# Optimization experiments

Measured on AMD Instinct MI355X. Metric: run time of the kernel, lower is better.

Reference implementation:

```python
import jax, jax.numpy as jnp
import numpy as np

DIM = 1024
N_HEAD = 16
HEAD_DIM = DIM // N_HEAD
SCALE = HEAD_DIM ** (-0.5)


def setup_inputs() -> dict:
    key = jax.random.key(0)
    ks = jax.random.split(key, 5)
    x = jax.random.normal(ks[0], (2, 2048, DIM), dtype=jnp.float32)
    # Linear params (torch nn.Linear stores weight as [out, in]; we keep [in, out])
    wqkv = jax.random.normal(ks[1], (DIM, 3 * DIM), dtype=jnp.float32) / np.sqrt(DIM)
    bqkv = jax.random.normal(ks[2], (3 * DIM,), dtype=jnp.float32) * 0.01
    wo = jax.random.normal(ks[3], (DIM, DIM), dtype=jnp.float32) / np.sqrt(DIM)
    bo = jax.random.normal(ks[4], (DIM,), dtype=jnp.float32) * 0.01
    return {"x": x, "wqkv": wqkv, "bqkv": bqkv, "wo": wo, "bo": bo}


def reference(x, wqkv, bqkv, wo, bo):
    b, s, _ = x.shape
    qkv = x @ wqkv + bqkv                      # [b, s, 3*dim]
    q, k, v = jnp.split(qkv, 3, axis=-1)
    # [b, s, h, d] -> [b, h, s, d]
    def heads(t):
        return t.reshape(b, s, N_HEAD, HEAD_DIM).transpose(0, 2, 1, 3)
    q, k, v = heads(q) * SCALE, heads(k), heads(v)
    attn = jnp.einsum('bhqd,bhkd->bhqk', q, k)  # [b, h, s, s]
    attn = jax.nn.softmax(attn, axis=-1)
    out = jnp.einsum('bhqk,bhkd->bhqd', attn, v)
    out = out.transpose(0, 2, 1, 3).reshape(b, s, DIM)
    return out @ wo + bo
```

## Files before the change

kernel.cpp:

```cpp
#include <hip/hip_runtime.h>
#include <hip/hip_bf16.h>

#define DIM   1024
#define NHEAD 16
#define HDIM  64
#define BATCH 2
#define SEQ   2048
#define TOK   (BATCH*SEQ)
#define QSCALE 0.1803368801111204f

typedef unsigned short u16;
typedef __attribute__((ext_vector_type(8))) _Float16 h16x8;
typedef __attribute__((ext_vector_type(2))) __fp16 fp16x2;
typedef __attribute__((ext_vector_type(4))) float f32x4;
typedef __attribute__((ext_vector_type(16))) float f32x16;
typedef __attribute__((ext_vector_type(2))) int i32x2;

__device__ __forceinline__ u16 f2h(float f) {
    union { _Float16 h; u16 u; } v; v.h = (_Float16)f;
    return v.u;
}
__device__ __forceinline__ unsigned pack2h(float a, float b) {
    return (unsigned)f2h(a) | ((unsigned)f2h(b) << 16);
}
__device__ __forceinline__ unsigned pkrtz(float a, float b) {
    union { fp16x2 h; unsigned u; } v;
    v.h = __builtin_amdgcn_cvt_pkrtz(a, b);
    return v.u;
}
__device__ __forceinline__ f32x16 zero16() {
    f32x16 v;
#pragma unroll
    for (int i = 0; i < 16; ++i) v[i] = 0.f;
    return v;
}

typedef __attribute__((address_space(3))) void lds_void;
typedef const __attribute__((address_space(1))) void gbl_void;
__device__ __forceinline__ void gload_lds16(const void* g, void* l) {
    __builtin_amdgcn_global_load_lds((gbl_void*)g, (lds_void*)l, 16, 0, 0);
}

__global__ __launch_bounds__(256)
void fused_cvt(const float* __restrict__ x,    u16* __restrict__ xh,
               const float* __restrict__ wqkv, u16* __restrict__ wqT,
               const float* __restrict__ wo,   u16* __restrict__ woT) {
    __shared__ float t[32][33];
    const int bid = blockIdx.x;
    if (bid < 4096) {
        int i = bid * 256 + threadIdx.x;
        float4 v = ((const float4*)x)[i];
        ((uint2*)xh)[i] = make_uint2(pack2h(v.x, v.y), pack2h(v.z, v.w));
        return;
    }
    const float* in; u16* outT; int K, N, tb;
    if (bid < 7168) { in = wqkv; outT = wqT; K = 1024; N = 3072; tb = bid - 4096; }
    else            { in = wo;   outT = woT; K = 1024; N = 1024; tb = bid - 7168; }
    const int nbx = N / 32;
    const int n0 = (tb % nbx) * 32, k0 = (tb / nbx) * 32;
    const int tx = threadIdx.x & 31, ty = threadIdx.x >> 5;
#pragma unroll
    for (int i = 0; i < 4; ++i)
        t[ty + i * 8][tx] = in[(size_t)(k0 + ty + i * 8) * N + n0 + tx];
    __syncthreads();
#pragma unroll
    for (int i = 0; i < 4; ++i)
        outT[(size_t)(n0 + ty + i * 8) * K + k0 + tx] = f2h(t[tx][ty + i * 8]);
}

__global__ __launch_bounds__(512)
void gemm_qkv(const u16* __restrict__ Ag, const u16* __restrict__ Bg,
              const float* __restrict__ bias, u16* __restrict__ Qh,
              u16* __restrict__ Kh, u16* __restrict__ Vh, int K, int N) {
    __shared__ u16 As[128 * 64];
    __shared__ u16 Bs[128 * 64];

    const int tid  = threadIdx.x;
    const int lane = tid & 63;
    const int w    = tid >> 6;
    const int c    = lane & 15;
    const int quad = lane >> 4;
    const int wm   = (w & 3) * 32;
    const int wn   = (w >> 2) * 64;
    const int row0 = blockIdx.y * 128;
    const int col0 = blockIdx.x * 128;
    const int sw   = c & 7;

    f32x4 acc[2][4];
#pragma unroll
    for (int m = 0; m < 2; ++m)
#pragma unroll
        for (int n = 0; n < 4; ++n) acc[m][n] = (f32x4){0.f, 0.f, 0.f, 0.f};

    for (int k0 = 0; k0 < K; k0 += 64) {
        __syncthreads();
#pragma unroll
        for (int i = 0; i < 2; ++i) {
            int idx = tid + i * 512;
            int r = idx >> 3, p = idx & 7;
            int g = p ^ (r & 7);
            gload_lds16(Ag + (size_t)(row0 + r) * K + k0 + g * 8, &As[idx * 8]);
            gload_lds16(Bg + (size_t)(col0 + r) * K + k0 + g * 8, &Bs[idx * 8]);
        }
        __syncthreads();

        h16x8 af[2][2];
#pragma unroll
        for (int m = 0; m < 2; ++m)
#pragma unroll
            for (int kh = 0; kh < 2; ++kh)
                af[m][kh] = *(const h16x8*)&As[(wm + m * 16 + c) * 64 +
                                              ((kh * 4 + quad) ^ sw) * 8];
#pragma unroll
        for (int kh = 0; kh < 2; ++kh)
#pragma unroll
            for (int n = 0; n < 4; ++n) {
                h16x8 bf = *(const h16x8*)&Bs[(wn + n * 16 + c) * 64 +
                                              ((kh * 4 + quad) ^ sw) * 8];
#pragma unroll
                for (int m = 0; m < 2; ++m)
                    acc[m][n] = __builtin_amdgcn_mfma_f32_16x16x32_f16(
                        af[m][kh], bf, acc[m][n], 0, 0, 0);
            }
    }

#pragma unroll
    for (int n = 0; n < 4; ++n) {
        const int col = col0 + wn + n * 16 + c;
        const float bv = bias[col];
        const int h = (col >> 6) & 15, d = col & 63;
#pragma unroll
        for (int m = 0; m < 2; ++m) {
            const int rbase = row0 + wm + m * 16 + quad * 4;
            const int b = rbase >> 11, s0 = rbase & (SEQ - 1);
            const int bh = (b << 4) + h;
            if (col0 < DIM) {
#pragma unroll
                for (int r = 0; r < 4; ++r)
                    Qh[((size_t)bh * SEQ + s0 + r) * 64 + d] =
                        f2h((acc[m][n][r] + bv) * QSCALE);
            } else if (col0 < 2 * DIM) {
#pragma unroll
                for (int r = 0; r < 4; ++r)
                    Kh[((size_t)bh * SEQ + s0 + r) * 64 + d] =
                        f2h(acc[m][n][r] + bv);
            } else {
                uint2 pv = make_uint2(pack2h(acc[m][n][0] + bv, acc[m][n][1] + bv),
                                      pack2h(acc[m][n][2] + bv, acc[m][n][3] + bv));
                *(uint2*)&Vh[((size_t)bh * 64 + d) * SEQ + s0] = pv;
            }
        }
    }
}

__global__ __launch_bounds__(512)
void gemm_out(const u16* __restrict__ Ag, const u16* __restrict__ Bg,
              const float* __restrict__ bias, float* __restrict__ Cout,
              int M, int N, int K) {
    __shared__ u16 As[128 * 64];
    __shared__ u16 Bs[128 * 64];

    const int tid  = threadIdx.x;
    const int lane = tid & 63;
    const int w    = tid >> 6;
    const int c    = lane & 15;
    const int quad = lane >> 4;
    const int wm   = (w & 3) * 32;
    const int wn   = (w >> 2) * 64;
    const int row0 = blockIdx.y * 128;
    const int col0 = blockIdx.x * 128;
    const int sw   = c & 7;

    f32x4 acc[2][4];
#pragma unroll
    for (int m = 0; m < 2; ++m)
#pragma unroll
        for (int n = 0; n < 4; ++n) acc[m][n] = (f32x4){0.f, 0.f, 0.f, 0.f};

    for (int k0 = 0; k0 < K; k0 += 64) {
        __syncthreads();
#pragma unroll
        for (int i = 0; i < 2; ++i) {
            int idx = tid + i * 512;
            int r = idx >> 3, p = idx & 7;
            int g = p ^ (r & 7);
            gload_lds16(Ag + (size_t)(row0 + r) * K + k0 + g * 8, &As[idx * 8]);
            gload_lds16(Bg + (size_t)(col0 + r) * K + k0 + g * 8, &Bs[idx * 8]);
        }
        __syncthreads();

        h16x8 af[2][2];
#pragma unroll
        for (int m = 0; m < 2; ++m)
#pragma unroll
            for (int kh = 0; kh < 2; ++kh)
                af[m][kh] = *(const h16x8*)&As[(wm + m * 16 + c) * 64 +
                                              ((kh * 4 + quad) ^ sw) * 8];
#pragma unroll
        for (int kh = 0; kh < 2; ++kh)
#pragma unroll
            for (int n = 0; n < 4; ++n) {
                h16x8 bf = *(const h16x8*)&Bs[(wn + n * 16 + c) * 64 +
                                              ((kh * 4 + quad) ^ sw) * 8];
#pragma unroll
                for (int m = 0; m < 2; ++m)
                    acc[m][n] = __builtin_amdgcn_mfma_f32_16x16x32_f16(
                        af[m][kh], bf, acc[m][n], 0, 0, 0);
            }
    }

#pragma unroll
    for (int n = 0; n < 4; ++n) {
        const int col = col0 + wn + n * 16 + c;
        const float bv = bias[col];
#pragma unroll
        for (int m = 0; m < 2; ++m) {
            const int rbase = row0 + wm + m * 16 + quad * 4;
#pragma unroll
            for (int r = 0; r < 4; ++r)
                Cout[(size_t)(rbase + r) * N + col] = acc[m][n][r] + bv;
        }
    }
}

__global__ __launch_bounds__(256, 2)
void flash_attn11(const u16* __restrict__ Qg, const u16* __restrict__ Kg,
                  const u16* __restrict__ Vg, u16* __restrict__ aout) {
    __shared__ u16 Qs[128 * 64];
    __shared__ u16 Ks[2][128 * 64];
    __shared__ u16 Vt[2][64 * 128];

    const int tid  = threadIdx.x;
    const int lane = tid & 63;
    const int w    = tid >> 6;
    const int wq   = w & 1;
    const int wk   = w >> 1;
    const int n32  = lane & 31;
    const int q5   = lane >> 5;
    const int bh   = blockIdx.y;
    const int q0   = blockIdx.x * 128;

    const u16* Qb = Qg + (size_t)bh * SEQ * 64;
    const u16* Kb = Kg + (size_t)bh * SEQ * 64;
    const u16* Vb = Vg + (size_t)bh * 64 * SEQ;

#pragma unroll
    for (int i = 0; i < 4; ++i) {
        int idx = tid + i * 256;
        int r = idx >> 3, p = idx & 7, g = p ^ (r & 7);
        gload_lds16(Qb + (size_t)(q0 + r) * 64 + g * 8, &Qs[idx * 8]);
    }
#pragma unroll
    for (int i = 0; i < 4; ++i) {
        int idx = tid + i * 256;
        int rk = idx >> 3, pk = idx & 7, gk = pk ^ (rk & 7);
        gload_lds16(Kb + (size_t)rk * 64 + gk * 8, &Ks[0][idx * 8]);
        int rv = idx >> 4, cv = idx & 15, gv = cv ^ (rv & 7);
        gload_lds16(Vb + (size_t)rv * SEQ + gv * 8, &Vt[0][idx * 8]);
    }
    __syncthreads();

    const int qrowA = wq * 64 + n32;
    const int qrowB = qrowA + 32;
    const int sw    = n32 & 7;
    h16x8 qbA[4], qbB[4];
#pragma unroll
    for (int s = 0; s < 4; ++s) {
        const int ch = ((s * 2 + q5) ^ sw) * 8;
        qbA[s] = *(const h16x8*)&Qs[qrowA * 64 + ch];
        qbB[s] = *(const h16x8*)&Qs[qrowB * 64 + ch];
    }

    float lA = 0.f, lB = 0.f;
    f32x16 oA[2] = {zero16(), zero16()};
    f32x16 oB[2] = {zero16(), zero16()};

    for (int kt = 0; kt < SEQ / 128; ++kt) {
        const int cur = kt & 1, nxt = cur ^ 1;

        if (kt < SEQ / 128 - 1) {
            const int k1 = (kt + 1) * 128;
#pragma unroll
            for (int i = 0; i < 4; ++i) {
                int idx = tid + i * 256;
                int rk = idx >> 3, pk = idx & 7, gk = pk ^ (rk & 7);
                gload_lds16(Kb + (size_t)(k1 + rk) * 64 + gk * 8, &Ks[nxt][idx * 8]);
                int rv = idx >> 4, cv = idx & 15, gv = cv ^ (rv & 7);
                gload_lds16(Vb + (size_t)rv * SEQ + k1 + gv * 8, &Vt[nxt][idx * 8]);
            }
        }

        unsigned xwA[8][2], xwB[8][2];
#pragma unroll
        for (int sub = 0; sub < 2; ++sub) {
            const int kr = wk * 64 + sub * 32 + n32;
            f32x16 saA = zero16(), saB = zero16();
            __builtin_amdgcn_s_setprio(1);
#pragma unroll
            for (int s = 0; s < 4; ++s) {
                h16x8 ak = *(const h16x8*)&Ks[cur][kr * 64 +
                                                   (((s * 2 + q5) ^ sw) * 8)];
                saA = __builtin_amdgcn_mfma_f32_32x32x16_f16(ak, qbA[s], saA, 0, 0, 0);
                saB = __builtin_amdgcn_mfma_f32_32x32x16_f16(ak, qbB[s], saB, 0, 0, 0);
            }
            __builtin_amdgcn_s_setprio(0);
#pragma unroll
            for (int rr = 0; rr < 4; ++rr) {
                float a0 = __builtin_amdgcn_exp2f(saA[4 * rr + 0]);
                float a1 = __builtin_amdgcn_exp2f(saA[4 * rr + 1]);
                float a2 = __builtin_amdgcn_exp2f(saA[4 * rr + 2]);
                float a3 = __builtin_amdgcn_exp2f(saA[4 * rr + 3]);
                lA += (a0 + a1) + (a2 + a3);
                xwA[sub * 4 + rr][0] = pkrtz(a0, a1);
                xwA[sub * 4 + rr][1] = pkrtz(a2, a3);
                float b0 = __builtin_amdgcn_exp2f(saB[4 * rr + 0]);
                float b1 = __builtin_amdgcn_exp2f(saB[4 * rr + 1]);
                float b2 = __builtin_amdgcn_exp2f(saB[4 * rr + 2]);
                float b3 = __builtin_amdgcn_exp2f(saB[4 * rr + 3]);
                lB += (b0 + b1) + (b2 + b3);
                xwB[sub * 4 + rr][0] = pkrtz(b0, b1);
                xwB[sub * 4 + rr][1] = pkrtz(b2, b3);
            }
        }

        h16x8 bpA[4], bpB[4];
#pragma unroll
        for (int s = 0; s < 4; ++s) {
            i32x2 ra = __builtin_amdgcn_permlane32_swap(
                (int)xwA[2 * s][0], (int)xwA[2 * s + 1][0], false, false);
            i32x2 rb = __builtin_amdgcn_permlane32_swap(
                (int)xwA[2 * s][1], (int)xwA[2 * s + 1][1], false, false);
            union { int u[4]; h16x8 h; } fa;
            fa.u[0] = ra[0]; fa.u[1] = rb[0]; fa.u[2] = ra[1]; fa.u[3] = rb[1];
            bpA[s] = fa.h;
            i32x2 rc = __builtin_amdgcn_permlane32_swap(
                (int)xwB[2 * s][0], (int)xwB[2 * s + 1][0], false, false);
            i32x2 rd = __builtin_amdgcn_permlane32_swap(
                (int)xwB[2 * s][1], (int)xwB[2 * s + 1][1], false, false);
            union { int u[4]; h16x8 h; } fb;
            fb.u[0] = rc[0]; fb.u[1] = rd[0]; fb.u[2] = rc[1]; fb.u[3] = rd[1];
            bpB[s] = fb.h;
        }

        __builtin_amdgcn_s_setprio(1);
#pragma unroll
        for (int dt = 0; dt < 2; ++dt) {
            const int dr = dt * 32 + n32;
#pragma unroll
            for (int s = 0; s < 4; ++s) {
                h16x8 av = *(const h16x8*)&Vt[cur][dr * 128 +
                                                   ((wk * 8 + ((s * 2 + q5) ^ sw)) * 8)];
                oA[dt] = __builtin_amdgcn_mfma_f32_32x32x16_f16(av, bpA[s], oA[dt], 0, 0, 0);
                oB[dt] = __builtin_amdgcn_mfma_f32_32x32x16_f16(av, bpB[s], oB[dt], 0, 0, 0);
            }
        }
        __builtin_amdgcn_s_setprio(0);

        __syncthreads();
    }

    lA += __shfl_xor(lA, 32, 64);
    lB += __shfl_xor(lB, 32, 64);

    float* oc = (float*)Vt;
    float* lc = (float*)Qs;
    const int rowA = (wq * 2 + 0) * 64 + lane;
    const int rowB = (wq * 2 + 1) * 64 + lane;
    if (wk == 1) {
#pragma unroll
        for (int dt = 0; dt < 2; ++dt)
#pragma unroll
            for (int i = 0; i < 16; ++i) {
                oc[rowA * 32 + ((dt * 16 + i + lane) & 31)] = oA[dt][i];
                oc[rowB * 32 + ((dt * 16 + i + lane) & 31)] = oB[dt][i];
            }
        lc[rowA] = lA;
        lc[rowB] = lB;
    }
    __syncthreads();
    if (wk == 1) return;
    lA += lc[rowA];
    lB += lc[rowB];
#pragma unroll
    for (int dt = 0; dt < 2; ++dt)
#pragma unroll
        for (int i = 0; i < 16; ++i) {
            oA[dt][i] += oc[rowA * 32 + ((dt * 16 + i + lane) & 31)];
            oB[dt][i] += oc[rowB * 32 + ((dt * 16 + i + lane) & 31)];
        }

    const float invA = 1.f / lA, invB = 1.f / lB;
    const int b = bh >> 4, h = bh & 15;
    const size_t roA = (size_t)(b * SEQ + q0 + qrowA) * DIM + h * HDIM;
    const size_t roB = (size_t)(b * SEQ + q0 + qrowB) * DIM + h * HDIM;
#pragma unroll
    for (int dt = 0; dt < 2; ++dt) {
#pragma unroll
        for (int rq = 0; rq < 4; ++rq) {
            const int d = dt * 32 + 8 * rq + 4 * q5;
            *(uint2*)&aout[roA + d] = make_uint2(
                pkrtz(oA[dt][4 * rq + 0] * invA, oA[dt][4 * rq + 1] * invA),
                pkrtz(oA[dt][4 * rq + 2] * invA, oA[dt][4 * rq + 3] * invA));
            *(uint2*)&aout[roB + d] = make_uint2(
                pkrtz(oB[dt][4 * rq + 0] * invB, oB[dt][4 * rq + 1] * invB),
                pkrtz(oB[dt][4 * rq + 2] * invB, oB[dt][4 * rq + 3] * invB));
        }
    }
}

extern "C" void kernel_launch(void* const* d_in, const int* in_sizes, int n_in,
                              void* d_out, int out_size, void* d_ws, size_t ws_size,
                              hipStream_t stream) {
    (void)in_sizes; (void)n_in; (void)out_size; (void)ws_size;
    const float* x    = (const float*)d_in[0];
    const float* wqkv = (const float*)d_in[1];
    const float* bqkv = (const float*)d_in[2];
    const float* wo   = (const float*)d_in[3];
    const float* bo   = (const float*)d_in[4];
    float* out = (float*)d_out;

    const size_t HB = (size_t)BATCH * NHEAD * SEQ * HDIM;
    u16* Qh  = (u16*)d_ws;
    u16* Kh  = Qh + HB;
    u16* Vh  = Kh + HB;
    u16* ao  = Vh + HB;
    u16* wqT = ao + (size_t)TOK * DIM;
    u16* woT = wqT + (size_t)3 * DIM * DIM;
    u16* xh  = woT + (size_t)DIM * DIM;

    fused_cvt<<<8192, 256, 0, stream>>>(x, xh, wqkv, wqT, wo, woT);
    gemm_qkv<<<dim3(3 * DIM / 128, TOK / 128), 512, 0, stream>>>(
        xh, wqT, bqkv, Qh, Kh, Vh, DIM, 3 * DIM);
    flash_attn11<<<dim3(SEQ / 128, BATCH * NHEAD), 256, 0, stream>>>(
        Qh, Kh, Vh, ao);
    gemm_out<<<dim3(DIM / 128, TOK / 128), 512, 0, stream>>>(
        ao, woT, bo, out, TOK, DIM, DIM);
}
```

Baseline: 177.3 us.

## Double-buffer output GEMM LDS loads and stage V transpose through shared memory

The output projection GEMM now keeps two LDS buffers and issues the next K-tile's global-to-LDS loads before computing on the current tile. This overlaps memory latency with MFMA work and removes one barrier per iteration, at the cost of twice the shared memory. Separately, the QKV GEMM's V epilogue now writes the tile transposed into a swizzled LDS buffer and then stores 16-byte contiguous rows to the transposed V layout. This replaces the scattered 8-byte stores of the old V path.

```diff
diff --git a/kernel.cpp b/kernel.cpp
--- a/kernel.cpp
+++ b/kernel.cpp
@@ -72,8 +72,9 @@
 void gemm_qkv(const u16* __restrict__ Ag, const u16* __restrict__ Bg,
               const float* __restrict__ bias, u16* __restrict__ Qh,
               u16* __restrict__ Kh, u16* __restrict__ Vh, int K, int N) {
-    __shared__ u16 As[128 * 64];
-    __shared__ u16 Bs[128 * 64];
+    __shared__ u16 SMEM[2 * 128 * 64];
+    u16* As = SMEM;
+    u16* Bs = SMEM + 128 * 64;
 
     const int tid  = threadIdx.x;
     const int lane = tid & 63;
@@ -124,31 +125,57 @@
             }
     }
 
-#pragma unroll
-    for (int n = 0; n < 4; ++n) {
-        const int col = col0 + wn + n * 16 + c;
-        const float bv = bias[col];
-        const int h = (col >> 6) & 15, d = col & 63;
-#pragma unroll
-        for (int m = 0; m < 2; ++m) {
-            const int rbase = row0 + wm + m * 16 + quad * 4;
-            const int b = rbase >> 11, s0 = rbase & (SEQ - 1);
-            const int bh = (b << 4) + h;
-            if (col0 < DIM) {
-#pragma unroll
-                for (int r = 0; r < 4; ++r)
-                    Qh[((size_t)bh * SEQ + s0 + r) * 64 + d] =
-                        f2h((acc[m][n][r] + bv) * QSCALE);
-            } else if (col0 < 2 * DIM) {
-#pragma unroll
-                for (int r = 0; r < 4; ++r)
-                    Kh[((size_t)bh * SEQ + s0 + r) * 64 + d] =
-                        f2h(acc[m][n][r] + bv);
-            } else {
-                uint2 pv = make_uint2(pack2h(acc[m][n][0] + bv, acc[m][n][1] + bv),
-                                      pack2h(acc[m][n][2] + bv, acc[m][n][3] + bv));
-                *(uint2*)&Vh[((size_t)bh * 64 + d) * SEQ + s0] = pv;
-            }
+    if (col0 < 2 * DIM) {
+#pragma unroll
+        for (int n = 0; n < 4; ++n) {
+            const int col = col0 + wn + n * 16 + c;
+            const float bv = bias[col];
+            const int h = (col >> 6) & 15, d = col & 63;
+#pragma unroll
+            for (int m = 0; m < 2; ++m) {
+                const int rbase = row0 + wm + m * 16 + quad * 4;
+                const int b = rbase >> 11, s0 = rbase & (SEQ - 1);
+                const int bh = (b << 4) + h;
+                if (col0 < DIM) {
+#pragma unroll
+                    for (int r = 0; r < 4; ++r)
+                        Qh[((size_t)bh * SEQ + s0 + r) * 64 + d] =
+                            f2h((acc[m][n][r] + bv) * QSCALE);
+                } else {
+#pragma unroll
+                    for (int r = 0; r < 4; ++r)
+                        Kh[((size_t)bh * SEQ + s0 + r) * 64 + d] =
+                            f2h(acc[m][n][r] + bv);
+                }
+            }
+        }
+    } else {
+        __syncthreads();
+        const int c8 = (c & 7) << 4;
+#pragma unroll
+        for (int n = 0; n < 4; ++n) {
+            const int tc = wn + n * 16 + c;
+            const float bv = bias[col0 + tc];
+#pragma unroll
+            for (int m = 0; m < 2; ++m) {
+                const int tr0 = wm + m * 16 + quad * 4;
+                *(uint2*)&SMEM[tc * 128 + (tr0 ^ c8)] = make_uint2(
+                    pack2h(acc[m][n][0] + bv, acc[m][n][1] + bv),
+                    pack2h(acc[m][n][2] + bv, acc[m][n][3] + bv));
+            }
+        }
+        __syncthreads();
+        const int b16  = (row0 >> 11) << 4;
+        const int srow = row0 & (SEQ - 1);
+#pragma unroll
+        for (int j = 0; j < 4; ++j) {
+            const int idx1d = tid + j * 512;
+            const int tc = idx1d >> 4, sc = idx1d & 15;
+            const int bh = b16 + (((col0 >> 6) + (tc >> 6)) & 15);
+            const int d  = tc & 63;
+            uint4 v = *(const uint4*)&SMEM[tc * 128 +
+                                           ((sc * 8) ^ ((tc & 7) << 4))];
+            *(uint4*)&Vh[((size_t)bh * 64 + d) * SEQ + srow + sc * 8] = v;
         }
     }
 }
@@ -157,8 +184,8 @@
 void gemm_out(const u16* __restrict__ Ag, const u16* __restrict__ Bg,
               const float* __restrict__ bias, float* __restrict__ Cout,
               int M, int N, int K) {
-    __shared__ u16 As[128 * 64];
-    __shared__ u16 Bs[128 * 64];
+    __shared__ u16 As[2][128 * 64];
+    __shared__ u16 Bs[2][128 * 64];
 
     const int tid  = threadIdx.x;
     const int lane = tid & 63;
@@ -171,42 +198,50 @@
     const int col0 = blockIdx.x * 128;
     const int sw   = c & 7;
 
-    f32x4 acc[2][4];
-#pragma unroll
-    for (int m = 0; m < 2; ++m)
-#pragma unroll
-        for (int n = 0; n < 4; ++n) acc[m][n] = (f32x4){0.f, 0.f, 0.f, 0.f};
-
-    for (int k0 = 0; k0 < K; k0 += 64) {
-        __syncthreads();
+    auto stage = [&](int buf, int koff) {
 #pragma unroll
         for (int i = 0; i < 2; ++i) {
             int idx = tid + i * 512;
             int r = idx >> 3, p = idx & 7;
             int g = p ^ (r & 7);
-            gload_lds16(Ag + (size_t)(row0 + r) * K + k0 + g * 8, &As[idx * 8]);
-            gload_lds16(Bg + (size_t)(col0 + r) * K + k0 + g * 8, &Bs[idx * 8]);
-        }
-        __syncthreads();
+            gload_lds16(Ag + (size_t)(row0 + r) * K + koff + g * 8, &As[buf][idx * 8]);
+            gload_lds16(Bg + (size_t)(col0 + r) * K + koff + g * 8, &Bs[buf][idx * 8]);
+        }
+    };
+
+    f32x4 acc[2][4];
+#pragma unroll
+    for (int m = 0; m < 2; ++m)
+#pragma unroll
+        for (int n = 0; n < 4; ++n) acc[m][n] = (f32x4){0.f, 0.f, 0.f, 0.f};
+
+    stage(0, 0);
+    __syncthreads();
+    int cur = 0;
+    for (int k0 = 0; k0 < K; k0 += 64) {
+        if (k0 + 64 < K) stage(cur ^ 1, k0 + 64);
 
         h16x8 af[2][2];
 #pragma unroll
         for (int m = 0; m < 2; ++m)
 #pragma unroll
             for (int kh = 0; kh < 2; ++kh)
-                af[m][kh] = *(const h16x8*)&As[(wm + m * 16 + c) * 64 +
-                                              ((kh * 4 + quad) ^ sw) * 8];
+                af[m][kh] = *(const h16x8*)&As[cur][(wm + m * 16 + c) * 64 +
+                                                   ((kh * 4 + quad) ^ sw) * 8];
 #pragma unroll
         for (int kh = 0; kh < 2; ++kh)
 #pragma unroll
             for (int n = 0; n < 4; ++n) {
-                h16x8 bf = *(const h16x8*)&Bs[(wn + n * 16 + c) * 64 +
-                                              ((kh * 4 + quad) ^ sw) * 8];
+                h16x8 bf = *(const h16x8*)&Bs[cur][(wn + n * 16 + c) * 64 +
+                                                   ((kh * 4 + quad) ^ sw) * 8];
 #pragma unroll
                 for (int m = 0; m < 2; ++m)
                     acc[m][n] = __builtin_amdgcn_mfma_f32_16x16x32_f16(
                         af[m][kh], bf, acc[m][n], 0, 0, 0);
             }
+
+        __syncthreads();
+        cur ^= 1;
     }
 
 #pragma unroll
```

Measured after the change: 182.2 us. +2.7%, slower.
